# Kernel tuning notes

Measured on AMD Instinct MI355X. Metric: run time of the kernel, lower is better.

Reference implementation:

```python
import jax, jax.numpy as jnp
import numpy as np

S = 768    # sequence length (residues)
CS = 384   # single_embedding_size
CP = 128   # pair_embedding_size
E = 16     # embedding_size per head
PQ = 4     # num_query_points
PV = 8     # num_value_points
H = 12     # num_heads


def setup_inputs() -> dict:
    key = jax.random.key(0)
    ks = jax.random.split(key, 14)

    def w(k, shape, scale=0.02):
        return jax.random.normal(k, shape, dtype=jnp.float32) * scale

    # Orthonormal rotation matrices per residue (proper rigid frames)
    rot_raw = jax.random.normal(ks[2], (S, 3, 3), dtype=jnp.float32)
    rotations, _ = jnp.linalg.qr(rot_raw)

    return {
        "single_representation": jax.random.normal(ks[0], (S, CS), dtype=jnp.float32),
        "pair_representation": jax.random.normal(ks[1], (S, S, CP), dtype=jnp.float32),
        "frames_rotations": rotations,
        "frames_translations": jax.random.normal(ks[3], (S, 3), dtype=jnp.float32),
        # learned parameters (layouts match the torch view() conventions)
        "Wq": w(ks[4], (H, E, CS)),
        "Wk": w(ks[5], (H, E, CS)),
        "Wv": w(ks[6], (H, E, CS)),
        "Wqp": w(ks[7], (H, PQ, 3, CS)),
        "Wkp": w(ks[8], (H, PQ, 3, CS)),
        "Wvp": w(ks[9], (H, PV, 3, CS)),
        "Wb": w(ks[10], (H, CP)),
        "Wo": w(ks[11], (CS, H * (CP + E + PV * 4))),
        "bo": jnp.zeros((CS,), dtype=jnp.float32),
        "gamma": jnp.ones((H,), dtype=jnp.float32),  # scale_head parameter
    }


def _frame_apply(R, t, x):
    # R: [S,3,3], t: [S,3], x: [H,S,P,3] -> R_s @ x + t_s per residue s
    return jnp.einsum('sij,hspj->hspi', R, x) + t[None, :, None, :]


def reference(single_representation, pair_representation, frames_rotations,
              frames_translations, Wq, Wk, Wv, Wqp, Wkp, Wvp, Wb, Wo, bo, gamma):
    s_len = single_representation.shape[0]
    e = Wq.shape[1]
    pq = Wqp.shape[1]
    scale_single = 1.0 / np.sqrt(e)
    scale_frame = -1.0 / np.sqrt(18.0 * pq)

    # --- attention logits from three sources ---
    q = jnp.einsum('hec,sc->hse', Wq, single_representation)
    k = jnp.einsum('hec,sc->hse', Wk, single_representation)
    w_single = scale_single * jnp.einsum('hie,hje->hij', q, k)          # [H,S,S]

    w_pair = jnp.einsum('hc,ijc->hij', Wb, pair_representation)          # [H,S,S]

    qp = jnp.einsum('hpdc,sc->hspd', Wqp, single_representation)         # [H,S,PQ,3]
    kp = jnp.einsum('hpdc,sc->hspd', Wkp, single_representation)
    lqp = _frame_apply(frames_rotations, frames_translations, qp)
    lkp = _frame_apply(frames_rotations, frames_translations, kp)
    diff = lqp[:, :, None, :, :] - lkp[:, None, :, :, :]                 # [H,S,S,PQ,3]
    w_frame = jnp.sum(diff * diff, axis=(-2, -1))                        # [H,S,S]
    w_frame = scale_frame * jax.nn.softplus(gamma)[:, None, None] * w_frame

    a = jax.nn.softmax(w_single + w_pair + w_frame, axis=-1)             # [H,S,S]

    # --- fan-out into three attention outputs ---
    v = jnp.einsum('hec,sc->hse', Wv, single_representation)
    o_single = jnp.einsum('hij,hje->ihe', a, v).reshape(s_len, -1)       # [S, H*E]

    # faithful to source: sum over the query dim of a, then contract keys
    a_sum = jnp.sum(a, axis=1)                                           # [H,S(keys)]
    o_pair = jnp.einsum('hk,ikc->ihc', a_sum, pair_representation).reshape(s_len, -1)

    vp = jnp.einsum('hpdc,sc->hspd', Wvp, single_representation)         # [H,S,PV,3]
    lvp = _frame_apply(frames_rotations, frames_translations, vp)
    o_local = jnp.einsum('hij,hjpd->hipd', a, lvp)                       # [H,S,PV,3]
    Rinv = jnp.swapaxes(frames_rotations, -1, -2)
    tinv = -jnp.einsum('sij,sj->si', Rinv, frames_translations)
    o_global = _frame_apply(Rinv, tinv, o_local)                         # [H,S,PV,3]
    o_pts = jnp.transpose(o_global, (1, 2, 0, 3)).reshape(s_len, -1)     # [S, PV*H*3]
    o_norm = jnp.transpose(jnp.linalg.norm(o_global, axis=-1), (1, 2, 0)).reshape(s_len, -1)

    attn = jnp.concatenate([o_single, o_pair, o_pts, o_norm], axis=-1)
    return attn @ Wo.T + bo
```

## Files before the change

kernel.cpp:

```cpp
#include <hip/hip_runtime.h>
#include <hip/hip_bf16.h>

#define S 768
#define CS 384
#define CP 128
#define E 16
#define PQ 4
#define PV 8
#define H 12
#define FDIM 2112
#define OFF_PAIR 192
#define OFF_PTS 1728
#define OFF_NORM 2016

typedef __hip_bfloat16 bf16;

__device__ __forceinline__ float b2f(bf16 x){ return __bfloat162float(x); }
__device__ __forceinline__ bf16 f2b(float x){ return __float2bfloat16(x); }
__device__ __forceinline__ float blo(unsigned u){ return __uint_as_float(u << 16); }
__device__ __forceinline__ float bhi(unsigned u){ return __uint_as_float(u & 0xffff0000u); }
__device__ __forceinline__ void up8(uint4 u, float* f){
  f[0]=blo(u.x); f[1]=bhi(u.x); f[2]=blo(u.y); f[3]=bhi(u.y);
  f[4]=blo(u.z); f[5]=bhi(u.z); f[6]=blo(u.w); f[7]=bhi(u.w);
}

__global__ __launch_bounds__(256) void k_proj_wpair(
    const float* __restrict__ sr, const float* __restrict__ rot, const float* __restrict__ trans,
    const float* __restrict__ Wq, const float* __restrict__ Wk, const float* __restrict__ Wv,
    const float* __restrict__ Wqp, const float* __restrict__ Wkp, const float* __restrict__ Wvp,
    float* __restrict__ q, float* __restrict__ k, float* __restrict__ vT,
    float* __restrict__ lqp, float* __restrict__ lkp, float* __restrict__ lvpT,
    const float* __restrict__ pair, const float* __restrict__ Wb, float* __restrict__ wp)
{
  if (blockIdx.x < S/2){
    int s0 = blockIdx.x*2;
    __shared__ float srs[2][CS];
    __shared__ float Rs[2][9];
    __shared__ float ts[2][3];
    for (int x = threadIdx.x; x < 2*CS; x += 256) ((float*)srs)[x] = sr[(size_t)s0*CS + x];
    if (threadIdx.x < 18) ((float*)Rs)[threadIdx.x] = rot[(size_t)s0*9 + threadIdx.x];
    if (threadIdx.x >= 64 && threadIdx.x < 70) ((float*)ts)[threadIdx.x-64] = trans[(size_t)s0*3 + threadIdx.x-64];
    __syncthreads();

    for (int task = threadIdx.x; task < 768; task += 256){
      if (task < 576){
        int which = task / 192;
        int he = task - which*192;
        int h = he >> 4, e = he & 15;
        const float* W = (which==0 ? Wq : (which==1 ? Wk : Wv)) + (size_t)he*CS;
        const float4* W4 = (const float4*)W;
        float acc[2] = {0.f,0.f};
        for (int cc = 0; cc < CS/4; ++cc){
          float4 w = W4[cc];
          #pragma unroll
          for (int r = 0; r < 2; ++r){
            const float* sp = srs[r] + cc*4;
            acc[r] += w.x*sp[0] + w.y*sp[1] + w.z*sp[2] + w.w*sp[3];
          }
        }
        #pragma unroll
        for (int r = 0; r < 2; ++r){
          int s = s0 + r;
          if (which == 0)      q[((size_t)h*S + s)*E + e] = acc[r];
          else if (which == 1) k[((size_t)h*S + s)*E + e] = acc[r];
          else                 vT[((size_t)h*E + e)*S + s] = acc[r];
        }
      } else {
        int pt = task - 576;
        int h = pt >> 4, slot = pt & 15;
        int kind, p; const float* W;
        if (slot < 4)      { kind = 0; p = slot;     W = Wqp + (size_t)((h*PQ+p)*3)*CS; }
        else if (slot < 8) { kind = 1; p = slot - 4; W = Wkp + (size_t)((h*PQ+p)*3)*CS; }
        else               { kind = 2; p = slot - 8; W = Wvp + (size_t)((h*PV+p)*3)*CS; }
        const float4* W0 = (const float4*)W;
        const float4* W1 = (const float4*)(W + CS);
        const float4* W2 = (const float4*)(W + 2*CS);
        float a0[2] = {0,0}, a1[2] = {0,0}, a2[2] = {0,0};
        for (int cc = 0; cc < CS/4; ++cc){
          float4 w0 = W0[cc], w1 = W1[cc], w2 = W2[cc];
          #pragma unroll
          for (int r = 0; r < 2; ++r){
            const float* sp = srs[r] + cc*4;
            a0[r] += w0.x*sp[0] + w0.y*sp[1] + w0.z*sp[2] + w0.w*sp[3];
            a1[r] += w1.x*sp[0] + w1.y*sp[1] + w1.z*sp[2] + w1.w*sp[3];
            a2[r] += w2.x*sp[0] + w2.y*sp[1] + w2.z*sp[2] + w2.w*sp[3];
          }
        }
        #pragma unroll
        for (int r = 0; r < 2; ++r){
          int s = s0 + r;
          float l0 = Rs[r][0]*a0[r] + Rs[r][1]*a1[r] + Rs[r][2]*a2[r] + ts[r][0];
          float l1 = Rs[r][3]*a0[r] + Rs[r][4]*a1[r] + Rs[r][5]*a2[r] + ts[r][1];
          float l2 = Rs[r][6]*a0[r] + Rs[r][7]*a1[r] + Rs[r][8]*a2[r] + ts[r][2];
          if (kind == 0){ float* d = lqp + ((size_t)h*S + s)*12 + p*3; d[0]=l0; d[1]=l1; d[2]=l2; }
          else if (kind == 1){ float* d = lkp + ((size_t)h*S + s)*12 + p*3; d[0]=l0; d[1]=l1; d[2]=l2; }
          else {
            float* dst = lvpT + (size_t)h*24*S;
            dst[(size_t)(p*3+0)*S + s] = l0;
            dst[(size_t)(p*3+1)*S + s] = l1;
            dst[(size_t)(p*3+2)*S + s] = l2;
          }
        }
      }
    }
  } else {
    int r = (blockIdx.x - S/2)*256 + threadIdx.x;
    const float4* prow = (const float4*)(pair + (size_t)r*CP);
    float acc[H];
    #pragma unroll
    for (int h = 0; h < H; ++h) acc[h] = 0.f;
    #pragma unroll
    for (int half = 0; half < 2; ++half){
      float4 buf[16];
      #pragma unroll
      for (int cc = 0; cc < 16; ++cc) buf[cc] = prow[half*16 + cc];
      #pragma unroll
      for (int h = 0; h < H; ++h){
        const float4* wb = (const float4*)(Wb + h*CP + half*64);
        float p0=0.f, p1=0.f, p2=0.f, p3=0.f;
        #pragma unroll
        for (int cc = 0; cc < 16; ++cc){
          float4 wv = wb[cc];
          p0 += wv.x*buf[cc].x; p1 += wv.y*buf[cc].y;
          p2 += wv.z*buf[cc].z; p3 += wv.w*buf[cc].w;
        }
        acc[h] += (p0+p1)+(p2+p3);
      }
    }
    #pragma unroll
    for (int h = 0; h < H; ++h) wp[(size_t)h*S*S + r] = acc[h];
  }
}

__global__ __launch_bounds__(256) void k_attn(
    const float* __restrict__ wp,
    const float* __restrict__ q, const float* __restrict__ k,
    const float* __restrict__ lqp, const float* __restrict__ lkp,
    const float* __restrict__ gamma, bf16* __restrict__ ab)
{
  int i    = blockIdx.x / 3;
  int hg   = blockIdx.x % 3;
  int lane = threadIdx.x & 63;
  int w    = __builtin_amdgcn_readfirstlane(threadIdx.x >> 6);
  int h    = hg*4 + w;

  __shared__ float lgs[4][S];

  const float* qrow = q   + ((size_t)h*S + i)*E;
  const float* lqr  = lqp + ((size_t)h*S + i)*12;
  const float* wrow = wp  + ((size_t)h*S + i)*S;
  float sf = -0.11785113019775793f * log1pf(__expf(gamma[h]));

  float qv[E];
  #pragma unroll
  for (int e = 0; e < E; ++e) qv[e] = qrow[e];
  float lq[12];
  #pragma unroll
  for (int x = 0; x < 12; ++x) lq[x] = lqr[x];

  float mloc = -1e30f;
  #pragma unroll 3
  for (int jj = 0; jj < 12; ++jj){
    int j = lane + jj*64;
    const float4* kr4 = (const float4*)(k   + ((size_t)h*S + j)*E);
    const float4* lk4 = (const float4*)(lkp + ((size_t)h*S + j)*12);
    float4 k0 = kr4[0], k1 = kr4[1], k2 = kr4[2], k3 = kr4[3];
    float4 p0 = lk4[0], p1 = lk4[1], p2 = lk4[2];
    float d = qv[0]*k0.x + qv[1]*k0.y + qv[2]*k0.z + qv[3]*k0.w
            + qv[4]*k1.x + qv[5]*k1.y + qv[6]*k1.z + qv[7]*k1.w
            + qv[8]*k2.x + qv[9]*k2.y + qv[10]*k2.z + qv[11]*k2.w
            + qv[12]*k3.x + qv[13]*k3.y + qv[14]*k3.z + qv[15]*k3.w;
    float d0 = lq[0]-p0.x, d1 = lq[1]-p0.y, d2  = lq[2]-p0.z,  d3  = lq[3]-p0.w;
    float d4 = lq[4]-p1.x, d5 = lq[5]-p1.y, d6  = lq[6]-p1.z,  d7  = lq[7]-p1.w;
    float d8 = lq[8]-p2.x, d9 = lq[9]-p2.y, d10 = lq[10]-p2.z, d11 = lq[11]-p2.w;
    float fr = d0*d0 + d1*d1 + d2*d2 + d3*d3 + d4*d4 + d5*d5
             + d6*d6 + d7*d7 + d8*d8 + d9*d9 + d10*d10 + d11*d11;
    float lg = wrow[j] + 0.25f*d + sf*fr;
    lgs[w][j] = lg;
    mloc = fmaxf(mloc, lg);
  }
  #pragma unroll
  for (int mk = 1; mk < 64; mk <<= 1) mloc = fmaxf(mloc, __shfl_xor(mloc, mk));

  float sum = 0.f;
  #pragma unroll 3
  for (int jj = 0; jj < 12; ++jj){
    int j = lane + jj*64;
    float v = __expf(lgs[w][j] - mloc);
    lgs[w][j] = v;
    sum += v;
  }
  #pragma unroll
  for (int mk = 1; mk < 64; mk <<= 1) sum += __shfl_xor(sum, mk);
  float inv = 1.f/sum;

  size_t base = ((size_t)h*S + i)*S;
  #pragma unroll 3
  for (int jj = 0; jj < 12; ++jj){
    int j = lane + jj*64;
    ab[base + j] = f2b(lgs[w][j]*inv);
  }
}

__global__ __launch_bounds__(256) void k_sv_asum(
    const bf16* __restrict__ ab, const float* __restrict__ vT, const float* __restrict__ lvpT,
    const float* __restrict__ rot, const float* __restrict__ trans,
    bf16* __restrict__ attnb, float* __restrict__ asumT)
{
  if (blockIdx.x < 384){
    int h  = blockIdx.x / 32;
    int i0 = (blockIdx.x % 32) * 24;
    int t  = threadIdx.x;
    float a0 = 0.f, a1 = 0.f, a2 = 0.f;
    for (int i = i0; i < i0 + 24; ++i){
      const bf16* row = ab + ((size_t)h*S + i)*S;
      a0 += b2f(row[t]);
      a1 += b2f(row[t + 256]);
      a2 += b2f(row[t + 512]);
    }
    atomicAdd(&asumT[(t      )*H + h], a0);
    atomicAdd(&asumT[(t + 256)*H + h], a1);
    atomicAdd(&asumT[(t + 512)*H + h], a2);
  } else {
    int bid  = blockIdx.x - 384;
    int h    = bid / (S/4);
    int i0   = (bid % (S/4))*4;
    int w    = threadIdx.x >> 6;
    int lane = threadIdx.x & 63;
    int i = i0 + w;
    const uint4* ar4 = (const uint4*)(ab + ((size_t)h*S + i)*S);
    float acc = 0.f;
    const float* src = nullptr;
    if (lane < 16)      src = vT   + ((size_t)h*E  + lane)*S;
    else if (lane < 40) src = lvpT + ((size_t)h*24 + (lane-16))*S;
    if (src){
      for (int jb = 0; jb < S/8; ++jb){
        float af[8]; up8(ar4[jb], af);
        float4 s0 = *(const float4*)(src + jb*8);
        float4 s1 = *(const float4*)(src + jb*8 + 4);
        acc += af[0]*s0.x + af[1]*s0.y + af[2]*s0.z + af[3]*s0.w
             + af[4]*s1.x + af[5]*s1.y + af[6]*s1.z + af[7]*s1.w;
      }
    }
    __shared__ float ol[4][24];
    __shared__ float ogs[4][24];
    int pd = lane - 16;
    if (lane >= 16 && lane < 40) ol[w][pd] = acc;
    __syncthreads();
    if (lane < 16){
      attnb[(size_t)i*FDIM + h*E + lane] = f2b(acc);
    } else if (lane < 40){
      int p = pd/3, d = pd%3;
      float r0 = rot[(size_t)i*9 + 0 + d];
      float r1 = rot[(size_t)i*9 + 3 + d];
      float r2 = rot[(size_t)i*9 + 6 + d];
      float x0 = ol[w][p*3+0] - trans[i*3+0];
      float x1 = ol[w][p*3+1] - trans[i*3+1];
      float x2 = ol[w][p*3+2] - trans[i*3+2];
      float og = r0*x0 + r1*x1 + r2*x2;
      attnb[(size_t)i*FDIM + OFF_PTS + p*(H*3) + h*3 + d] = f2b(og);
      ogs[w][pd] = og;
    }
    __syncthreads();
    if (lane >= 16 && lane < 40 && (pd % 3) == 0){
      int p = pd/3;
      float g0 = ogs[w][p*3], g1 = ogs[w][p*3+1], g2 = ogs[w][p*3+2];
      attnb[(size_t)i*FDIM + OFF_NORM + p*H + h] = f2b(sqrtf(g0*g0 + g1*g1 + g2*g2));
    }
  }
}

__global__ __launch_bounds__(512) void k_opair(const float* __restrict__ pair,
                                               const float* __restrict__ asumT,
                                               bf16* __restrict__ attnb)
{
  int i  = blockIdx.x;
  int t  = threadIdx.x;
  int c2 = t & 63;
  int g  = __builtin_amdgcn_readfirstlane(t >> 6);
  float accx[H], accy[H];
  #pragma unroll
  for (int h = 0; h < H; ++h){ accx[h] = 0.f; accy[h] = 0.f; }
  const float2* prow = (const float2*)(pair + (size_t)i*S*CP) + c2;
  for (int kk = 0; kk < 96; ++kk){
    int kj = g*96 + kk;
    float2 pv = prow[(size_t)kj*64];
    const float* ap = asumT + kj*H;
    #pragma unroll
    for (int h = 0; h < H; ++h){
      accx[h] += ap[h]*pv.x;
      accy[h] += ap[h]*pv.y;
    }
  }
  __shared__ float part[8][H][CP];
  #pragma unroll
  for (int h = 0; h < H; ++h)
    ((float2*)part[g][h])[c2] = make_float2(accx[h], accy[h]);
  __syncthreads();
  if (t < CP){
    #pragma unroll
    for (int h = 0; h < H; ++h){
      float s = part[0][h][t] + part[1][h][t] + part[2][h][t] + part[3][h][t]
              + part[4][h][t] + part[5][h][t] + part[6][h][t] + part[7][h][t];
      attnb[(size_t)i*FDIM + OFF_PAIR + h*CP + t] = f2b(s);
    }
  }
}

__global__ __launch_bounds__(384) void k_final(const bf16* __restrict__ attnb,
                                               const float* __restrict__ Wo,
                                               const float* __restrict__ bo,
                                               float* __restrict__ out)
{
  int i0 = blockIdx.x*4;
  int ck = blockIdx.y;
  int o  = threadIdx.x;
  const float4* wrow = (const float4*)(Wo + (size_t)o*FDIM) + ck*132;
  const unsigned* a0 = (const unsigned*)(attnb + (size_t)i0*FDIM) + ck*264;
  const unsigned* a1 = a0 + FDIM/2;
  const unsigned* a2 = a1 + FDIM/2;
  const unsigned* a3 = a2 + FDIM/2;
  float c0=0.f, c1=0.f, c2=0.f, c3=0.f;
  for (int cc = 0; cc < 132; ++cc){
    float4 wv = wrow[cc];
    unsigned u;
    u = a0[cc*2]; c0 += wv.x*blo(u)+wv.y*bhi(u); u = a0[cc*2+1]; c0 += wv.z*blo(u)+wv.w*bhi(u);
    u = a1[cc*2]; c1 += wv.x*blo(u)+wv.y*bhi(u); u = a1[cc*2+1]; c1 += wv.z*blo(u)+wv.w*bhi(u);
    u = a2[cc*2]; c2 += wv.x*blo(u)+wv.y*bhi(u); u = a2[cc*2+1]; c2 += wv.z*blo(u)+wv.w*bhi(u);
    u = a3[cc*2]; c3 += wv.x*blo(u)+wv.y*bhi(u); u = a3[cc*2+1]; c3 += wv.z*blo(u)+wv.w*bhi(u);
  }
  if (ck == 0){
    float b = bo[o];
    c0 += b; c1 += b; c2 += b; c3 += b;
  }
  atomicAdd(&out[(size_t)(i0+0)*CS + o], c0);
  atomicAdd(&out[(size_t)(i0+1)*CS + o], c1);
  atomicAdd(&out[(size_t)(i0+2)*CS + o], c2);
  atomicAdd(&out[(size_t)(i0+3)*CS + o], c3);
}

extern "C" void kernel_launch(void* const* d_in, const int* in_sizes, int n_in,
                              void* d_out, int out_size, void* d_ws, size_t ws_size,
                              hipStream_t stream)
{
  const float* sr    = (const float*)d_in[0];
  const float* pair  = (const float*)d_in[1];
  const float* rot   = (const float*)d_in[2];
  const float* trans = (const float*)d_in[3];
  const float* Wq    = (const float*)d_in[4];
  const float* Wk    = (const float*)d_in[5];
  const float* Wv    = (const float*)d_in[6];
  const float* Wqp   = (const float*)d_in[7];
  const float* Wkp   = (const float*)d_in[8];
  const float* Wvp   = (const float*)d_in[9];
  const float* Wb    = (const float*)d_in[10];
  const float* Wo    = (const float*)d_in[11];
  const float* bo    = (const float*)d_in[12];
  const float* gamma = (const float*)d_in[13];

  float* ws    = (float*)d_ws;
  float* q     = ws;
  float* k     = q     + 147456;
  float* vT    = k     + 147456;
  float* lqp   = vT    + 147456;
  float* lkp   = lqp   + 110592;
  float* lvpT  = lkp   + 110592;
  float* asumT = lvpT  + 221184;
  bf16*  ab    = (bf16*)(asumT + 9216);
  bf16*  attnb = (bf16*)(asumT + 9216 + 3538944);
  float* wp    = asumT + 9216 + 3538944 + 811008;
  float* out = (float*)d_out;

  hipMemsetAsync(asumT, 0, (size_t)S*H*sizeof(float), stream);
  hipMemsetAsync(out,   0, (size_t)S*CS*sizeof(float), stream);
  k_proj_wpair<<<S/2 + (S*S)/256, 256, 0, stream>>>(sr, rot, trans, Wq, Wk, Wv, Wqp, Wkp, Wvp,
                                                    q, k, vT, lqp, lkp, lvpT, pair, Wb, wp);
  k_attn      <<<S*3,             256, 0, stream>>>(wp, q, k, lqp, lkp, gamma, ab);
  k_sv_asum   <<<384 + H*(S/4),   256, 0, stream>>>(ab, vT, lvpT, rot, trans, attnb, asumT);
  k_opair     <<<S,               512, 0, stream>>>(pair, asumT, attnb);
  k_final     <<<dim3(S/4, 4),    384, 0, stream>>>(attnb, Wo, bo, out);
}
```

Baseline: 880.0 us.

## Transpose key tensors and pack values as bf16 pairs for coalesced access

Keys and key points are now stored transposed (feature-major), so in the logits kernel each lane reads consecutive addresses across j instead of strided rows. Values and value points are packed as bf16 pairs interleaved by key position into a 48-wide row per key pair, with zero padding. The AV kernel then reads them coalesced across lanes and halves their bytes. This trades some precision on the values (now bf16) and adds padding-zeroing writes, in exchange for less memory traffic and better coalescing in the two attention kernels.

Result: faster. 750.8 us (-14.7%).

```diff
diff --git a/kernel.cpp b/kernel.cpp
--- a/kernel.cpp
+++ b/kernel.cpp
@@ -19,21 +19,27 @@
 __device__ __forceinline__ bf16 f2b(float x){ return __float2bfloat16(x); }
 __device__ __forceinline__ float blo(unsigned u){ return __uint_as_float(u << 16); }
 __device__ __forceinline__ float bhi(unsigned u){ return __uint_as_float(u & 0xffff0000u); }
-__device__ __forceinline__ void up8(uint4 u, float* f){
-  f[0]=blo(u.x); f[1]=bhi(u.x); f[2]=blo(u.y); f[3]=bhi(u.y);
-  f[4]=blo(u.z); f[5]=bhi(u.z); f[6]=blo(u.w); f[7]=bhi(u.w);
+__device__ __forceinline__ unsigned pk2(float a, float b){
+  bf16 x = f2b(a), y = f2b(b);
+  unsigned short ux = *reinterpret_cast<unsigned short*>(&x);
+  unsigned short uy = *reinterpret_cast<unsigned short*>(&y);
+  return (unsigned)ux | ((unsigned)uy << 16);
 }
 
 __global__ __launch_bounds__(256) void k_proj_wpair(
     const float* __restrict__ sr, const float* __restrict__ rot, const float* __restrict__ trans,
     const float* __restrict__ Wq, const float* __restrict__ Wk, const float* __restrict__ Wv,
     const float* __restrict__ Wqp, const float* __restrict__ Wkp, const float* __restrict__ Wvp,
-    float* __restrict__ q, float* __restrict__ k, float* __restrict__ vT,
-    float* __restrict__ lqp, float* __restrict__ lkp, float* __restrict__ lvpT,
+    float* __restrict__ q, float* __restrict__ kT, unsigned* __restrict__ vf2,
+    float* __restrict__ lqp, float* __restrict__ lkpT,
     const float* __restrict__ pair, const float* __restrict__ Wb, float* __restrict__ wp)
 {
   if (blockIdx.x < S/2){
     int s0 = blockIdx.x*2;
+    if (threadIdx.x < 96){
+      int hh = threadIdx.x >> 3, c = 40 + (threadIdx.x & 7);
+      vf2[((size_t)hh*(S/2) + blockIdx.x)*48 + c] = 0u;
+    }
     __shared__ float srs[2][CS];
     __shared__ float Rs[2][9];
     __shared__ float ts[2][3];
@@ -58,12 +64,14 @@
             acc[r] += w.x*sp[0] + w.y*sp[1] + w.z*sp[2] + w.w*sp[3];
           }
         }
-        #pragma unroll
-        for (int r = 0; r < 2; ++r){
-          int s = s0 + r;
-          if (which == 0)      q[((size_t)h*S + s)*E + e] = acc[r];
-          else if (which == 1) k[((size_t)h*S + s)*E + e] = acc[r];
-          else                 vT[((size_t)h*E + e)*S + s] = acc[r];
+        if (which == 0){
+          #pragma unroll
+          for (int r = 0; r < 2; ++r) q[((size_t)h*S + s0+r)*E + e] = acc[r];
+        } else if (which == 1){
+          #pragma unroll
+          for (int r = 0; r < 2; ++r) kT[((size_t)h*E + e)*S + s0+r] = acc[r];
+        } else {
+          vf2[((size_t)h*(S/2) + (s0>>1))*48 + e] = pk2(acc[0], acc[1]);
         }
       } else {
         int pt = task - 576;
@@ -86,6 +94,7 @@
             a2[r] += w2.x*sp[0] + w2.y*sp[1] + w2.z*sp[2] + w2.w*sp[3];
           }
         }
+        float lv[2][3];
         #pragma unroll
         for (int r = 0; r < 2; ++r){
           int s = s0 + r;
@@ -93,13 +102,20 @@
           float l1 = Rs[r][3]*a0[r] + Rs[r][4]*a1[r] + Rs[r][5]*a2[r] + ts[r][1];
           float l2 = Rs[r][6]*a0[r] + Rs[r][7]*a1[r] + Rs[r][8]*a2[r] + ts[r][2];
           if (kind == 0){ float* d = lqp + ((size_t)h*S + s)*12 + p*3; d[0]=l0; d[1]=l1; d[2]=l2; }
-          else if (kind == 1){ float* d = lkp + ((size_t)h*S + s)*12 + p*3; d[0]=l0; d[1]=l1; d[2]=l2; }
-          else {
-            float* dst = lvpT + (size_t)h*24*S;
+          else if (kind == 1){
+            float* dst = lkpT + (size_t)h*12*S;
             dst[(size_t)(p*3+0)*S + s] = l0;
             dst[(size_t)(p*3+1)*S + s] = l1;
             dst[(size_t)(p*3+2)*S + s] = l2;
+          } else {
+            lv[r][0]=l0; lv[r][1]=l1; lv[r][2]=l2;
           }
+        }
+        if (kind == 2){
+          size_t base = ((size_t)h*(S/2) + (s0>>1))*48 + 16 + p*3;
+          vf2[base+0] = pk2(lv[0][0], lv[1][0]);
+          vf2[base+1] = pk2(lv[0][1], lv[1][1]);
+          vf2[base+2] = pk2(lv[0][2], lv[1][2]);
         }
       }
     }
@@ -134,8 +150,8 @@
 
 __global__ __launch_bounds__(256) void k_attn(
     const float* __restrict__ wp,
-    const float* __restrict__ q, const float* __restrict__ k,
-    const float* __restrict__ lqp, const float* __restrict__ lkp,
+    const float* __restrict__ q, const float* __restrict__ kT,
+    const float* __restrict__ lqp, const float* __restrict__ lkpT,
     const float* __restrict__ gamma, bf16* __restrict__ ab)
 {
   int i    = blockIdx.x / 3;
@@ -149,6 +165,8 @@
   const float* qrow = q   + ((size_t)h*S + i)*E;
   const float* lqr  = lqp + ((size_t)h*S + i)*12;
   const float* wrow = wp  + ((size_t)h*S + i)*S;
+  const float* kTh  = kT   + (size_t)h*E*S;
+  const float* lkTh = lkpT + (size_t)h*12*S;
   float sf = -0.11785113019775793f * log1pf(__expf(gamma[h]));
 
   float qv[E];
@@ -159,22 +177,15 @@
   for (int x = 0; x < 12; ++x) lq[x] = lqr[x];
 
   float mloc = -1e30f;
-  #pragma unroll 3
+  #pragma unroll 2
   for (int jj = 0; jj < 12; ++jj){
     int j = lane + jj*64;
-    const float4* kr4 = (const float4*)(k   + ((size_t)h*S + j)*E);
-    const float4* lk4 = (const float4*)(lkp + ((size_t)h*S + j)*12);
-    float4 k0 = kr4[0], k1 = kr4[1], k2 = kr4[2], k3 = kr4[3];
-    float4 p0 = lk4[0], p1 = lk4[1], p2 = lk4[2];
-    float d = qv[0]*k0.x + qv[1]*k0.y + qv[2]*k0.z + qv[3]*k0.w
-            + qv[4]*k1.x + qv[5]*k1.y + qv[6]*k1.z + qv[7]*k1.w
-            + qv[8]*k2.x + qv[9]*k2.y + qv[10]*k2.z + qv[11]*k2.w
-            + qv[12]*k3.x + qv[13]*k3.y + qv[14]*k3.z + qv[15]*k3.w;
-    float d0 = lq[0]-p0.x, d1 = lq[1]-p0.y, d2  = lq[2]-p0.z,  d3  = lq[3]-p0.w;
-    float d4 = lq[4]-p1.x, d5 = lq[5]-p1.y, d6  = lq[6]-p1.z,  d7  = lq[7]-p1.w;
-    float d8 = lq[8]-p2.x, d9 = lq[9]-p2.y, d10 = lq[10]-p2.z, d11 = lq[11]-p2.w;
-    float fr = d0*d0 + d1*d1 + d2*d2 + d3*d3 + d4*d4 + d5*d5
-             + d6*d6 + d7*d7 + d8*d8 + d9*d9 + d10*d10 + d11*d11;
+    float d = 0.f;
+    #pragma unroll
+    for (int e = 0; e < E; ++e) d += qv[e]*kTh[(size_t)e*S + j];
+    float fr = 0.f;
+    #pragma unroll
+    for (int x = 0; x < 12; ++x){ float df = lq[x] - lkTh[(size_t)x*S + j]; fr += df*df; }
     float lg = wrow[j] + 0.25f*d + sf*fr;
     lgs[w][j] = lg;
     mloc = fmaxf(mloc, lg);
@@ -203,7 +214,7 @@
 }
 
 __global__ __launch_bounds__(256) void k_sv_asum(
-    const bf16* __restrict__ ab, const float* __restrict__ vT, const float* __restrict__ lvpT,
+    const bf16* __restrict__ ab, const unsigned* __restrict__ vf2,
     const float* __restrict__ rot, const float* __restrict__ trans,
     bf16* __restrict__ attnb, float* __restrict__ asumT)
 {
@@ -228,19 +239,19 @@
     int w    = threadIdx.x >> 6;
     int lane = threadIdx.x & 63;
     int i = i0 + w;
-    const uint4* ar4 = (const uint4*)(ab + ((size_t)h*S + i)*S);
+    const unsigned* arow = (const unsigned*)(ab + ((size_t)h*S + i)*S);
     float acc = 0.f;
-    const float* src = nullptr;
-    if (lane < 16)      src = vT   + ((size_t)h*E  + lane)*S;
-    else if (lane < 40) src = lvpT + ((size_t)h*24 + (lane-16))*S;
-    if (src){
-      for (int jb = 0; jb < S/8; ++jb){
-        float af[8]; up8(ar4[jb], af);
-        float4 s0 = *(const float4*)(src + jb*8);
-        float4 s1 = *(const float4*)(src + jb*8 + 4);
-        acc += af[0]*s0.x + af[1]*s0.y + af[2]*s0.z + af[3]*s0.w
-             + af[4]*s1.x + af[5]*s1.y + af[6]*s1.z + af[7]*s1.w;
+    if (lane < 48){
+      const unsigned* vrow = vf2 + (size_t)h*(S/2)*48 + lane;
+      float acc1 = 0.f;
+      #pragma unroll 4
+      for (int jp = 0; jp < S/2; jp += 2){
+        unsigned ap0 = arow[jp], ap1 = arow[jp+1];
+        unsigned vp0 = vrow[(size_t)jp*48], vp1 = vrow[(size_t)(jp+1)*48];
+        acc  += blo(ap0)*blo(vp0) + bhi(ap0)*bhi(vp0);
+        acc1 += blo(ap1)*blo(vp1) + bhi(ap1)*bhi(vp1);
       }
+      acc += acc1;
     }
     __shared__ float ol[4][24];
     __shared__ float ogs[4][24];
@@ -359,24 +370,23 @@
   const float* gamma = (const float*)d_in[13];
 
   float* ws    = (float*)d_ws;
-  float* q     = ws;
-  float* k     = q     + 147456;
-  float* vT    = k     + 147456;
-  float* lqp   = vT    + 147456;
-  float* lkp   = lqp   + 110592;
-  float* lvpT  = lkp   + 110592;
-  float* asumT = lvpT  + 221184;
-  bf16*  ab    = (bf16*)(asumT + 9216);
-  bf16*  attnb = (bf16*)(asumT + 9216 + 3538944);
-  float* wp    = asumT + 9216 + 3538944 + 811008;
+  float*    q     = ws;
+  float*    kT    = q    + 147456;
+  float*    lqp   = kT   + 147456;
+  float*    lkpT  = lqp  + 110592;
+  unsigned* vf2   = (unsigned*)(lkpT + 110592);
+  float*    asumT = (float*)(vf2 + 221184);
+  bf16*     ab    = (bf16*)(asumT + 9216);
+  bf16*     attnb = (bf16*)(asumT + 9216 + 3538944);
+  float*    wp    = asumT + 9216 + 3538944 + 811008;
   float* out = (float*)d_out;
 
   hipMemsetAsync(asumT, 0, (size_t)S*H*sizeof(float), stream);
   hipMemsetAsync(out,   0, (size_t)S*CS*sizeof(float), stream);
   k_proj_wpair<<<S/2 + (S*S)/256, 256, 0, stream>>>(sr, rot, trans, Wq, Wk, Wv, Wqp, Wkp, Wvp,
-                                                    q, k, vT, lqp, lkp, lvpT, pair, Wb, wp);
-  k_attn      <<<S*3,             256, 0, stream>>>(wp, q, k, lqp, lkp, gamma, ab);
-  k_sv_asum   <<<384 + H*(S/4),   256, 0, stream>>>(ab, vT, lvpT, rot, trans, attnb, asumT);
+                                                    q, kT, vf2, lqp, lkpT, pair, Wb, wp);
+  k_attn      <<<S*3,             256, 0, stream>>>(wp, q, kT, lqp, lkpT, gamma, ab);
+  k_sv_asum   <<<384 + H*(S/4),   256, 0, stream>>>(ab, vf2, rot, trans, attnb, asumT);
   k_opair     <<<S,               512, 0, stream>>>(pair, asumT, attnb);
   k_final     <<<dim3(S/4, 4),    384, 0, stream>>>(attnb, Wo, bo, out);
 }
```
